# Kernel optimization log

Hardware: AMD Instinct MI355X
Metric: run time of the kernel (lower is better)

The kernel has to match this reference:

```python
import jax, jax.numpy as jnp
import numpy as np

B, S, D_IN, D_OUT = 4, 2048, 4096, 4096
NNZ = 167772


def setup_inputs() -> dict:
    key = jax.random.key(0)
    k_x, k_w, k_b, k_v, k_r, k_c = jax.random.split(key, 6)
    x = jax.random.normal(k_x, (B, S, D_IN), dtype=jnp.float32)
    W = jax.random.normal(k_w, (D_OUT, D_IN), dtype=jnp.float32) * 0.02
    b = jax.random.normal(k_b, (D_OUT,), dtype=jnp.float32) * 0.01
    delta_vals = jax.random.normal(k_v, (NNZ,), dtype=jnp.float32) * 0.01
    delta_rows = jax.random.randint(k_r, (NNZ,), 0, D_OUT)
    delta_cols = jax.random.randint(k_c, (NNZ,), 0, D_IN)
    return {"x": x, "W": W, "b": b, "delta_vals": delta_vals,
            "delta_rows": delta_rows, "delta_cols": delta_cols}


def reference(x, W, b, delta_vals, delta_rows, delta_cols):
    # output_sparse = pruned nn.Linear(x)
    out_sparse = jnp.einsum('bsi,oi->bso', x, W) + b
    # delta_B_csr as dense [out, in] built by scatter-add (duplicate coords sum, like CSR assembly)
    delta = jnp.zeros((D_OUT, D_IN), dtype=jnp.float32).at[delta_rows, delta_cols].add(delta_vals)
    # torch.sparse.mm(delta, x2d.T).T == x2d @ delta.T, computed in fp32
    comp = jnp.einsum('bsi,oi->bso', x.astype(jnp.float32), delta).astype(x.dtype)
    return out_sparse + comp
```

## Files before the change

kernel.cpp:

```cpp
#include <hip/hip_runtime.h>
#include <hip/hip_bf16.h>
#include <stdint.h>

#define B_    4
#define S_    2048
#define DIN   4096
#define DOUT  4096
#define NNZ_  167772
#define M_    (B_*S_)

typedef __attribute__((ext_vector_type(4))) float f32x4;
typedef __attribute__((ext_vector_type(8))) short s16x8;
typedef __attribute__((ext_vector_type(8))) unsigned short u16x8;

__device__ __forceinline__ unsigned short f2bf(float f) {
    unsigned int u = __float_as_uint(f);
    u += 0x7FFFu + ((u >> 16) & 1u);
    return (unsigned short)(u >> 16);
}

__device__ __forceinline__ void gload16(const void* g, void* l) {
    __builtin_amdgcn_global_load_lds(
        (const __attribute__((address_space(1))) unsigned int*)g,
        (__attribute__((address_space(3))) unsigned int*)l,
        16, 0, 0);
}


__global__ void zero_kernel(float* __restrict__ p, int n4) {
    int i = blockIdx.x * blockDim.x + threadIdx.x;
    if (i < n4) reinterpret_cast<f32x4*>(p)[i] = f32x4{0.f, 0.f, 0.f, 0.f};
}

__global__ void scatter_kernel(const float* __restrict__ vals,
                               const int* __restrict__ rows,
                               const int* __restrict__ cols,
                               float* __restrict__ delta, int nnz) {
    int i = blockIdx.x * blockDim.x + threadIdx.x;
    if (i < nnz) atomicAdd(delta + (size_t)rows[i] * DIN + cols[i], vals[i]);
}

__global__ void fuse_w_kernel(const float* __restrict__ W,
                              const float* __restrict__ delta,
                              unsigned short* __restrict__ Wb, int n8) {
    int i = blockIdx.x * blockDim.x + threadIdx.x;
    if (i >= n8) return;
    const f32x4* w4 = reinterpret_cast<const f32x4*>(W);
    const f32x4* d4 = reinterpret_cast<const f32x4*>(delta);
    f32x4 a0 = w4[2*i], a1 = w4[2*i+1];
    f32x4 b0 = d4[2*i], b1 = d4[2*i+1];
    u16x8 o;
    o[0]=f2bf(a0[0]+b0[0]); o[1]=f2bf(a0[1]+b0[1]); o[2]=f2bf(a0[2]+b0[2]); o[3]=f2bf(a0[3]+b0[3]);
    o[4]=f2bf(a1[0]+b1[0]); o[5]=f2bf(a1[1]+b1[1]); o[6]=f2bf(a1[2]+b1[2]); o[7]=f2bf(a1[3]+b1[3]);
    reinterpret_cast<u16x8*>(Wb)[i] = o;
}

__global__ void cvt_x_kernel(const float* __restrict__ x,
                             unsigned short* __restrict__ xb, int n8) {
    int i = blockIdx.x * blockDim.x + threadIdx.x;
    if (i >= n8) return;
    const f32x4* x4 = reinterpret_cast<const f32x4*>(x);
    f32x4 a0 = x4[2*i], a1 = x4[2*i+1];
    u16x8 o;
    o[0]=f2bf(a0[0]); o[1]=f2bf(a0[1]); o[2]=f2bf(a0[2]); o[3]=f2bf(a0[3]);
    o[4]=f2bf(a1[0]); o[5]=f2bf(a1[1]); o[6]=f2bf(a1[2]); o[7]=f2bf(a1[3]);
    reinterpret_cast<u16x8*>(xb)[i] = o;
}


__global__ __launch_bounds__(512, 2) void gemm_kernel(
    const unsigned short* __restrict__ A,
    const unsigned short* __restrict__ Bw,
    const float* __restrict__ bias,
    float* __restrict__ C)
{
    constexpr int K  = DIN;
    constexpr int N  = DOUT;
    constexpr int KB = K * 2;
    extern __shared__ char smem[];

    const int tid  = threadIdx.x;
    const int wave = tid >> 6;
    const int lane = tid & 63;
    const int wr = wave >> 2;
    const int wc = wave & 3;
    const int l16 = lane & 15;
    const int kq  = lane >> 4;
    const int s7  = l16 & 7;

    const int wg  = blockIdx.x;
    const int swz = (wg & 7) * 64 + (wg >> 3);
    const int bx  = swz & 15;
    const int by  = swz >> 4;
    const int rowBase = by * 256;
    const int colBase = bx * 256;

    const int r0    = tid >> 3;
    const int gslot = (tid & 7) ^ (r0 & 7);
    const char* gA = (const char*)A  + (size_t)(rowBase + r0) * KB + gslot * 16;
    const char* gB = (const char*)Bw + (size_t)(colBase + r0) * KB + gslot * 16;
    const int wvoff = wave * 1024;

    const unsigned q0 = (unsigned)(kq ^ s7);
    const unsigned q1 = (unsigned)((4 + kq) ^ s7);
    const unsigned aBase = (unsigned)((wr * 128 + l16) * 128);
    const unsigned bBase = (unsigned)((wc * 64  + l16) * 128);
    const unsigned short* aPtr[2][2];
    const unsigned short* bPtr[2][2];
    #pragma unroll
    for (int p_ = 0; p_ < 2; ++p_) {
        aPtr[p_][0] = (const unsigned short*)(smem + p_ * 65536 + aBase + q0 * 16);
        aPtr[p_][1] = (const unsigned short*)(smem + p_ * 65536 + aBase + q1 * 16);
        bPtr[p_][0] = (const unsigned short*)(smem + p_ * 65536 + 32768 + bBase + q0 * 16);
        bPtr[p_][1] = (const unsigned short*)(smem + p_ * 65536 + 32768 + bBase + q1 * 16);
    }

    f32x4 acc[8][4];
    #pragma unroll
    for (int i = 0; i < 8; ++i)
        #pragma unroll
        for (int j = 0; j < 4; ++j) acc[i][j] = f32x4{0.f, 0.f, 0.f, 0.f};

#define STAGE_A(P, T, H) do { \
    const char* g_ = gA + (size_t)(T) * 128 + (size_t)(H) * 1048576; \
    gload16(g_,          smem + (P) * 65536 + (H) * 16384 + wvoff); \
    gload16(g_ + 524288, smem + (P) * 65536 + (H) * 16384 + 8192 + wvoff); \
} while (0)

#define STAGE_B(P, T, H) do { \
    const char* g_ = gB + (size_t)(T) * 128 + (size_t)(H) * 1048576; \
    gload16(g_,          smem + (P) * 65536 + 32768 + (H) * 16384 + wvoff); \
    gload16(g_ + 524288, smem + (P) * 65536 + 32768 + (H) * 16384 + 8192 + wvoff); \
} while (0)

#define BAR() asm volatile("s_barrier" ::: "memory")

#define TILE(P, T, SB, SA, VN) do { \
    s16x8 af0[4][2], af1[4][2], bf0[2][2], bf1[2][2]; \
     \
    _Pragma("unroll") \
    for (int m_ = 0; m_ < 4; ++m_) { \
        af0[m_][0] = *(const s16x8*)(aPtr[P][0] + m_ * 1024); \
        af0[m_][1] = *(const s16x8*)(aPtr[P][1] + m_ * 1024); } \
    _Pragma("unroll") \
    for (int n_ = 0; n_ < 2; ++n_) { \
        bf0[n_][0] = *(const s16x8*)(bPtr[P][0] + n_ * 1024); \
        bf0[n_][1] = *(const s16x8*)(bPtr[P][1] + n_ * 1024); } \
    if (SB) STAGE_B(1 - (P), (T) + 1, 0); \
    BAR(); \
    __builtin_amdgcn_s_setprio(1); \
    _Pragma("unroll") \
    for (int m_ = 0; m_ < 4; ++m_) \
      _Pragma("unroll") \
      for (int n_ = 0; n_ < 2; ++n_) { \
        acc[m_][n_] = __builtin_amdgcn_mfma_f32_16x16x32_bf16(af0[m_][0], bf0[n_][0], acc[m_][n_], 0, 0, 0); \
        acc[m_][n_] = __builtin_amdgcn_mfma_f32_16x16x32_bf16(af0[m_][1], bf0[n_][1], acc[m_][n_], 0, 0, 0); } \
    __builtin_amdgcn_s_setprio(0); \
    BAR(); \
     \
    _Pragma("unroll") \
    for (int m_ = 0; m_ < 4; ++m_) { \
        af1[m_][0] = *(const s16x8*)(aPtr[P][0] + 4096 + m_ * 1024); \
        af1[m_][1] = *(const s16x8*)(aPtr[P][1] + 4096 + m_ * 1024); } \
    if (SB) STAGE_B(1 - (P), (T) + 1, 1); \
    BAR(); \
    __builtin_amdgcn_s_setprio(1); \
    _Pragma("unroll") \
    for (int m_ = 0; m_ < 4; ++m_) \
      _Pragma("unroll") \
      for (int n_ = 0; n_ < 2; ++n_) { \
        acc[4 + m_][n_] = __builtin_amdgcn_mfma_f32_16x16x32_bf16(af1[m_][0], bf0[n_][0], acc[4 + m_][n_], 0, 0, 0); \
        acc[4 + m_][n_] = __builtin_amdgcn_mfma_f32_16x16x32_bf16(af1[m_][1], bf0[n_][1], acc[4 + m_][n_], 0, 0, 0); } \
    __builtin_amdgcn_s_setprio(0); \
    BAR(); \
     \
    _Pragma("unroll") \
    for (int n_ = 0; n_ < 2; ++n_) { \
        bf1[n_][0] = *(const s16x8*)(bPtr[P][0] + 2048 + n_ * 1024); \
        bf1[n_][1] = *(const s16x8*)(bPtr[P][1] + 2048 + n_ * 1024); } \
    if (SA) STAGE_A(P, (T) + 2, 0); \
    BAR(); \
    __builtin_amdgcn_s_setprio(1); \
    _Pragma("unroll") \
    for (int m_ = 0; m_ < 4; ++m_) \
      _Pragma("unroll") \
      for (int n_ = 0; n_ < 2; ++n_) { \
        acc[m_][2 + n_] = __builtin_amdgcn_mfma_f32_16x16x32_bf16(af0[m_][0], bf1[n_][0], acc[m_][2 + n_], 0, 0, 0); \
        acc[m_][2 + n_] = __builtin_amdgcn_mfma_f32_16x16x32_bf16(af0[m_][1], bf1[n_][1], acc[m_][2 + n_], 0, 0, 0); } \
    __builtin_amdgcn_s_setprio(0); \
    BAR(); \
     \
    if (SA) STAGE_A(P, (T) + 2, 1); \
    BAR(); \
    __builtin_amdgcn_s_setprio(1); \
    _Pragma("unroll") \
    for (int m_ = 0; m_ < 4; ++m_) \
      _Pragma("unroll") \
      for (int n_ = 0; n_ < 2; ++n_) { \
        acc[4 + m_][2 + n_] = __builtin_amdgcn_mfma_f32_16x16x32_bf16(af1[m_][0], bf1[n_][0], acc[4 + m_][2 + n_], 0, 0, 0); \
        acc[4 + m_][2 + n_] = __builtin_amdgcn_mfma_f32_16x16x32_bf16(af1[m_][1], bf1[n_][1], acc[4 + m_][2 + n_], 0, 0, 0); } \
    __builtin_amdgcn_s_setprio(0); \
     \
    if (VN) { asm volatile("s_waitcnt vmcnt(4)" ::: "memory"); } \
    else    { asm volatile("s_waitcnt vmcnt(0)" ::: "memory"); } \
    BAR(); \
} while (0)

    STAGE_A(0, 0, 0); STAGE_A(0, 0, 1);
    STAGE_B(0, 0, 0); STAGE_B(0, 0, 1);
    STAGE_A(1, 1, 0); STAGE_A(1, 1, 1);
    asm volatile("s_waitcnt vmcnt(4)" ::: "memory");
    BAR();

    #pragma unroll 1
    for (int t = 0; t < 62; t += 2) {
        TILE(0, t,     1, 1, 4);
        TILE(1, t + 1, 1, 1, 4);
    }
    TILE(0, 62, 1, 0, 0);
    TILE(1, 63, 0, 0, 0);

#undef TILE
#undef BAR
#undef STAGE_A
#undef STAGE_B

    float bv[4];
    #pragma unroll
    for (int nf = 0; nf < 4; ++nf)
        bv[nf] = bias[colBase + wc * 64 + nf * 16 + l16];

    #pragma unroll
    for (int mf = 0; mf < 8; ++mf) {
        const int rowG = rowBase + wr * 128 + mf * 16 + kq * 4;
        float* cp = C + (size_t)rowG * N + colBase + wc * 64 + l16;
        #pragma unroll
        for (int nf = 0; nf < 4; ++nf)
            #pragma unroll
            for (int j = 0; j < 4; ++j)
                cp[(size_t)j * N + nf * 16] = acc[mf][nf][j] + bv[nf];
    }
}

extern "C" void kernel_launch(void* const* d_in, const int* in_sizes, int n_in,
                              void* d_out, int out_size, void* d_ws, size_t ws_size,
                              hipStream_t stream) {
    const float* x     = (const float*)d_in[0];
    const float* W     = (const float*)d_in[1];
    const float* b     = (const float*)d_in[2];
    const float* dvals = (const float*)d_in[3];
    const int*   drows = (const int*)d_in[4];
    const int*   dcols = (const int*)d_in[5];
    float* out = (float*)d_out;

    char* ws = (char*)d_ws;
    float*          delta = (float*)ws;
    unsigned short* Wb    = (unsigned short*)(ws + (size_t)64 * 1024 * 1024);
    unsigned short* xb    = (unsigned short*)(ws + (size_t)96 * 1024 * 1024);

    int n4 = DOUT * DIN / 4;
    zero_kernel<<<n4 / 256, 256, 0, stream>>>(delta, n4);
    scatter_kernel<<<(NNZ_ + 255) / 256, 256, 0, stream>>>(dvals, drows, dcols, delta, NNZ_);
    int n8w = DOUT * DIN / 8;
    fuse_w_kernel<<<n8w / 256, 256, 0, stream>>>(W, delta, Wb, n8w);
    int n8x = M_ * DIN / 8;
    cvt_x_kernel<<<n8x / 256, 256, 0, stream>>>(x, xb, n8x);

    static bool attr_done = false;
    if (!attr_done) {
        (void)hipFuncSetAttribute(reinterpret_cast<const void*>(gemm_kernel),
                                  hipFuncAttributeMaxDynamicSharedMemorySize, 131072);
        attr_done = true;
    }
    gemm_kernel<<<dim3(512), dim3(512), 131072, stream>>>(xb, Wb, b, out);
}
```

Before: 294.5 us.

## Scatter delta directly into bf16 weights and merge conversion kernels

Removes the dense fp32 delta matrix: no more zeroing 64MB, atomic scatter into it, and re-reading it during the W fuse. W and x are now converted to bf16 in one combined kernel, and the sparse corrections are added straight into the bf16 weights with a 32-bit CAS loop on the half-word. This cuts preprocessing memory traffic and two launches. The cost is extra rounding, since each correction is added in bf16 instead of fp32, and CAS retries wherever indices collide.

```diff
diff --git a/kernel.cpp b/kernel.cpp
--- a/kernel.cpp
+++ b/kernel.cpp
@@ -19,6 +19,10 @@
     return (unsigned short)(u >> 16);
 }
 
+__device__ __forceinline__ float bf2f(unsigned short h) {
+    return __uint_as_float(((unsigned int)h) << 16);
+}
+
 __device__ __forceinline__ void gload16(const void* g, void* l) {
     __builtin_amdgcn_global_load_lds(
         (const __attribute__((address_space(1))) unsigned int*)g,
@@ -27,44 +31,45 @@
 }
 
 
-__global__ void zero_kernel(float* __restrict__ p, int n4) {
+__global__ void cvt_both_kernel(const float* __restrict__ W,
+                                const float* __restrict__ x,
+                                unsigned short* __restrict__ Wb,
+                                unsigned short* __restrict__ xb,
+                                int n8w, int n8x) {
     int i = blockIdx.x * blockDim.x + threadIdx.x;
-    if (i < n4) reinterpret_cast<f32x4*>(p)[i] = f32x4{0.f, 0.f, 0.f, 0.f};
-}
-
-__global__ void scatter_kernel(const float* __restrict__ vals,
-                               const int* __restrict__ rows,
-                               const int* __restrict__ cols,
-                               float* __restrict__ delta, int nnz) {
-    int i = blockIdx.x * blockDim.x + threadIdx.x;
-    if (i < nnz) atomicAdd(delta + (size_t)rows[i] * DIN + cols[i], vals[i]);
-}
-
-__global__ void fuse_w_kernel(const float* __restrict__ W,
-                              const float* __restrict__ delta,
-                              unsigned short* __restrict__ Wb, int n8) {
-    int i = blockIdx.x * blockDim.x + threadIdx.x;
-    if (i >= n8) return;
-    const f32x4* w4 = reinterpret_cast<const f32x4*>(W);
-    const f32x4* d4 = reinterpret_cast<const f32x4*>(delta);
-    f32x4 a0 = w4[2*i], a1 = w4[2*i+1];
-    f32x4 b0 = d4[2*i], b1 = d4[2*i+1];
-    u16x8 o;
-    o[0]=f2bf(a0[0]+b0[0]); o[1]=f2bf(a0[1]+b0[1]); o[2]=f2bf(a0[2]+b0[2]); o[3]=f2bf(a0[3]+b0[3]);
-    o[4]=f2bf(a1[0]+b1[0]); o[5]=f2bf(a1[1]+b1[1]); o[6]=f2bf(a1[2]+b1[2]); o[7]=f2bf(a1[3]+b1[3]);
-    reinterpret_cast<u16x8*>(Wb)[i] = o;
-}
-
-__global__ void cvt_x_kernel(const float* __restrict__ x,
-                             unsigned short* __restrict__ xb, int n8) {
-    int i = blockIdx.x * blockDim.x + threadIdx.x;
-    if (i >= n8) return;
-    const f32x4* x4 = reinterpret_cast<const f32x4*>(x);
-    f32x4 a0 = x4[2*i], a1 = x4[2*i+1];
+    const float* src;
+    unsigned short* dst;
+    int j;
+    if (i < n8w) { src = W; dst = Wb; j = i; }
+    else         { src = x; dst = xb; j = i - n8w; if (j >= n8x) return; }
+    const f32x4* s4 = reinterpret_cast<const f32x4*>(src);
+    f32x4 a0 = s4[2*j], a1 = s4[2*j+1];
     u16x8 o;
     o[0]=f2bf(a0[0]); o[1]=f2bf(a0[1]); o[2]=f2bf(a0[2]); o[3]=f2bf(a0[3]);
     o[4]=f2bf(a1[0]); o[5]=f2bf(a1[1]); o[6]=f2bf(a1[2]); o[7]=f2bf(a1[3]);
-    reinterpret_cast<u16x8*>(xb)[i] = o;
+    reinterpret_cast<u16x8*>(dst)[j] = o;
+}
+
+__global__ void scatter_bf16_kernel(const float* __restrict__ vals,
+                                    const int* __restrict__ rows,
+                                    const int* __restrict__ cols,
+                                    unsigned short* __restrict__ Wb, int nnz) {
+    int i = blockIdx.x * blockDim.x + threadIdx.x;
+    if (i >= nnz) return;
+    size_t cell = (size_t)rows[i] * DIN + cols[i];
+    unsigned int* word = reinterpret_cast<unsigned int*>(Wb) + (cell >> 1);
+    const bool hiHalf = (cell & 1) != 0;
+    const float v = vals[i];
+    unsigned int old = *word, assumed;
+    do {
+        assumed = old;
+        unsigned short h = hiHalf ? (unsigned short)(assumed >> 16)
+                                  : (unsigned short)(assumed & 0xFFFFu);
+        unsigned short nh = f2bf(bf2f(h) + v);
+        unsigned int nw = hiHalf ? ((assumed & 0x0000FFFFu) | ((unsigned int)nh << 16))
+                                 : ((assumed & 0xFFFF0000u) | (unsigned int)nh);
+        old = atomicCAS(word, assumed, nw);
+    } while (old != assumed);
 }
 
 
@@ -254,17 +259,14 @@
     float* out = (float*)d_out;
 
     char* ws = (char*)d_ws;
-    float*          delta = (float*)ws;
-    unsigned short* Wb    = (unsigned short*)(ws + (size_t)64 * 1024 * 1024);
-    unsigned short* xb    = (unsigned short*)(ws + (size_t)96 * 1024 * 1024);
-
-    int n4 = DOUT * DIN / 4;
-    zero_kernel<<<n4 / 256, 256, 0, stream>>>(delta, n4);
-    scatter_kernel<<<(NNZ_ + 255) / 256, 256, 0, stream>>>(dvals, drows, dcols, delta, NNZ_);
+    unsigned short* Wb = (unsigned short*)ws;
+    unsigned short* xb = (unsigned short*)(ws + (size_t)32 * 1024 * 1024);
+
     int n8w = DOUT * DIN / 8;
-    fuse_w_kernel<<<n8w / 256, 256, 0, stream>>>(W, delta, Wb, n8w);
     int n8x = M_ * DIN / 8;
-    cvt_x_kernel<<<n8x / 256, 256, 0, stream>>>(x, xb, n8x);
+    int nblk = (n8w + n8x) / 256;
+    cvt_both_kernel<<<nblk, 256, 0, stream>>>(W, x, Wb, xb, n8w, n8x);
+    scatter_bf16_kernel<<<(NNZ_ + 255) / 256, 256, 0, stream>>>(dvals, drows, dcols, Wb, NNZ_);
 
     static bool attr_done = false;
     if (!attr_done) {
```

Measured after the change: 275.6 us. 1.07x faster.
